# Kernel tuning notes

Hardware: AMD Instinct MI355X
Metric: run time of the kernel (lower is better)

The kernel has to match this reference:

```python
import jax, jax.numpy as jnp
import numpy as np

B, T, D, H = 8, 4096, 1024, 8
BW = D // H
MIN_DECAY = 0.001
EPS = 1e-05        # RGLRU eps (clamps)
SCAN_EPS = 1e-07   # closed_form_rnn_scan eps


def setup_inputs() -> dict:
    key = jax.random.key(0)
    k0, k1, k2 = jax.random.split(key, 3)
    x = jax.random.normal(k0, (B, T, D), dtype=jnp.float32)
    a_param = jnp.full((D,), -3.0, dtype=jnp.float32)
    # block-diagonal gate params (orthogonal-ish init approximated by scaled normal)
    w_in = jax.random.normal(k1, (H, BW, BW), dtype=jnp.float32) * (1.0 / np.sqrt(BW))
    b_in = jnp.ones((H, BW), dtype=jnp.float32)
    w_a = jax.random.normal(k2, (H, BW, BW), dtype=jnp.float32) * (1.0 / np.sqrt(BW))
    b_a = jnp.ones((H, BW), dtype=jnp.float32)
    return {"x": x, "a_param": a_param, "w_in": w_in, "b_in": b_in, "w_a": w_a, "b_a": b_a}


def block_diag_linear(x, w, b):
    # x: [B,T,D] -> [B,T,H,BW] ; w: [H,BW,BW] ; b: [H,BW]
    xb = x.reshape(x.shape[:-1] + (H, BW))
    y = jnp.einsum('bthi,hij->bthj', xb, w) + b
    return y.reshape(x.shape)


def closed_form_rnn_scan(x, a):
    # x, a: [B,T,D]; h0 = 0
    a_cumprod = jnp.cumprod(a, axis=1)
    ones = jnp.ones((x.shape[0], 1, x.shape[2]), dtype=x.dtype)
    p_prefix = jnp.concatenate([ones, a_cumprod[:, :-1, :]], axis=1)
    p_prefix = jnp.maximum(p_prefix, SCAN_EPS)
    w = (x + SCAN_EPS) / p_prefix
    S = jnp.cumsum(w, axis=1)
    h = p_prefix * S  # + p_prefix * h0 with h0 = 0
    return h, h[:, -1, :]


def reference(x, a_param, w_in, b_in, w_a, b_a):
    gate_x = jax.nn.sigmoid(block_diag_linear(x, w_in, b_in))
    gate_a = jax.nn.sigmoid(block_diag_linear(x, w_a, b_a))
    log_a = -gate_a * (jax.nn.softplus(a_param) + MIN_DECAY)
    a = jnp.minimum(jnp.exp(log_a), 1.0 - EPS)
    gated_x = x * gate_x
    multiplier = jnp.sqrt(jnp.maximum(1.0 - a * a, EPS))
    normed_x = gated_x * multiplier
    h, _ = closed_form_rnn_scan(normed_x, a)
    return h
```

## Files before the change

kernel.cpp:

```cpp
#include <hip/hip_runtime.h>

#define B_ 8
#define T_ 4096
#define D_ 1024
#define H_ 8
#define BW_ 128
#define NC_ 32
#define CT_ 128
#define EPS7 1e-7f
#define EPS5 1e-5f
#define LOG1MEPS -1.0000186e-05f

typedef _Float16 f16x8 __attribute__((ext_vector_type(8)));
typedef _Float16 f16x4 __attribute__((ext_vector_type(4)));
typedef float f32x4 __attribute__((ext_vector_type(4)));

__global__ __launch_bounds__(256) void k1_gates(
    const float* __restrict__ x, const float* __restrict__ a_param,
    const float* __restrict__ w_in, const float* __restrict__ b_in,
    const float* __restrict__ w_a, const float* __restrict__ b_a,
    float* __restrict__ Abuf, float* __restrict__ NX, float* __restrict__ CS)
{
  const int bid  = blockIdx.x;
  const int kc   = bid & (NC_ - 1);
  const int h    = (bid >> 5) & (H_ - 1);
  const int b    = bid >> 8;
  const int tid  = threadIdx.x;
  const int wave = tid >> 6;
  const int lane = tid & 63;
  const int quad = lane >> 4;
  const int l15  = lane & 15;

  __shared__ _Float16 xs[128 * 136];

  const float* xg = x + (size_t)(b * T_ + kc * CT_) * D_ + h * BW_;
  const int jc = wave * 32;

  f16x8 bf[2][2][4];
  #pragma unroll
  for (int g = 0; g < 2; ++g) {
    const float* wptr = (g ? w_a : w_in) + h * BW_ * BW_;
    #pragma unroll
    for (int jt = 0; jt < 2; ++jt) {
      #pragma unroll
      for (int k = 0; k < 4; ++k) {
        const float* wp = wptr + (k * 32 + quad * 8) * BW_ + jc + jt * 16 + l15;
        f16x8 f;
        #pragma unroll
        for (int i = 0; i < 8; ++i) f[i] = (_Float16)wp[i * BW_];
        bf[g][jt][k] = f;
      }
    }
  }
  float bI[2], bA[2], cdec[2];
  #pragma unroll
  for (int jt = 0; jt < 2; ++jt) {
    const int j = h * BW_ + jc + jt * 16 + l15;
    bI[jt] = b_in[j];
    bA[jt] = b_a[j];
    const float ap = a_param[j];
    cdec[jt] = ((ap > 20.f) ? ap : log1pf(__expf(ap))) + 0.001f;
  }

  {
    const int row = tid >> 1;
    const int cb  = (tid & 1) * 64;
    #pragma unroll
    for (int i = 0; i < 16; ++i) {
      const float4 v = *(const float4*)(xg + row * D_ + cb + i * 4);
      f16x4 hv = { (_Float16)v.x, (_Float16)v.y, (_Float16)v.z, (_Float16)v.w };
      *(f16x4*)(xs + row * 136 + cb + i * 4) = hv;
    }
  }
  __syncthreads();

  f32x4 acc[2][2][8];
  #pragma unroll
  for (int g = 0; g < 2; ++g)
    #pragma unroll
    for (int jt = 0; jt < 2; ++jt)
      #pragma unroll
      for (int m = 0; m < 8; ++m)
        acc[g][jt][m] = (f32x4){0.f, 0.f, 0.f, 0.f};

  #pragma unroll
  for (int m = 0; m < 8; ++m) {
    f16x8 af[4];
    #pragma unroll
    for (int k = 0; k < 4; ++k)
      af[k] = *(const f16x8*)(xs + (m * 16 + l15) * 136 + k * 32 + quad * 8);
    #pragma unroll
    for (int k = 0; k < 4; ++k)
      #pragma unroll
      for (int g = 0; g < 2; ++g)
        #pragma unroll
        for (int jt = 0; jt < 2; ++jt)
          acc[g][jt][m] = __builtin_amdgcn_mfma_f32_16x16x32_f16(
              af[k], bf[g][jt][k], acc[g][jt][m], 0, 0, 0);
  }

  float sla[2] = {0.f, 0.f};
  const size_t obase = (size_t)(b * T_ + kc * CT_) * D_ + h * BW_;
  #pragma unroll
  for (int m = 0; m < 8; ++m) {
    #pragma unroll
    for (int r = 0; r < 4; ++r) {
      const int row = m * 16 + quad * 4 + r;
      #pragma unroll
      for (int jt = 0; jt < 2; ++jt) {
        const int col = jc + jt * 16 + l15;
        const float yi = acc[0][jt][m][r] + bI[jt];
        const float ya = acc[1][jt][m][r] + bA[jt];
        const float gx = __builtin_amdgcn_rcpf(1.f + __expf(-yi));
        const float ga = __builtin_amdgcn_rcpf(1.f + __expf(-ya));
        const float la = -ga * cdec[jt];
        const float a  = fminf(__expf(la), 1.0f - EPS5);
        const float mult = sqrtf(fmaxf(fmaf(-a, a, 1.0f), EPS5));
        const float xval = xg[row * D_ + col];
        const float nx = xval * gx * mult;
        const size_t gi = obase + (size_t)row * D_ + col;
        Abuf[gi] = a;
        NX[gi]   = nx;
        sla[jt] += fminf(la, LOG1MEPS);
      }
    }
  }
  #pragma unroll
  for (int jt = 0; jt < 2; ++jt) {
    sla[jt] += __shfl_xor(sla[jt], 16, 64);
    sla[jt] += __shfl_xor(sla[jt], 32, 64);
  }
  if (quad == 0) {
    const int cs = (b * NC_ + kc) * D_ + h * BW_ + jc;
    CS[cs + l15]      = sla[0];
    CS[cs + 16 + l15] = sla[1];
  }
}

__global__ __launch_bounds__(256) void k2_scan_logs(float* __restrict__ CS)
{
  const int idx = blockIdx.x * 256 + threadIdx.x;
  const int b = idx >> 10;
  const int d = idx & (D_ - 1);
  float lq = 0.f;
  #pragma unroll
  for (int kk = 0; kk < NC_; ++kk) {
    const int o = (b * NC_ + kk) * D_ + d;
    const float c = CS[o];
    CS[o] = lq;
    lq += c;
  }
}

__device__ __forceinline__ float scan_r(float c, float pp, float aprev) {
  return (c > EPS7) ? aprev
                    : ((pp > EPS7) ? (EPS7 * __builtin_amdgcn_rcpf(pp)) : 1.0f);
}

__global__ __launch_bounds__(256) void k3_summary(
    const float* __restrict__ Abuf, const float* __restrict__ NX,
    const float* __restrict__ LQ, float* __restrict__ Ak, float* __restrict__ Bk)
{
  const int bid = blockIdx.x;
  const int g = bid & 3;
  const int k = (bid >> 2) & (NC_ - 1);
  const int b = bid >> 7;
  const int d = g * 256 + threadIdx.x;
  const int t0 = k * CT_;
  const size_t base = (size_t)(b * T_ + t0) * D_ + d;

  float c, pp, aprev;
  if (k == 0) { c = 1.f; pp = 1.f; aprev = 1.f; }
  else {
    c = __expf(LQ[(b * NC_ + k) * D_ + d]);
    aprev = Abuf[base - D_];
    pp = fmaxf(c / aprev, EPS7);
  }
  float hv = 0.f, rp = 1.f;
  for (int t = 0; t < CT_; t += 8) {
    float av[8], uv[8];
    #pragma unroll
    for (int i = 0; i < 8; ++i) {
      av[i] = Abuf[base + (size_t)(t + i) * D_];
      uv[i] = NX[base + (size_t)(t + i) * D_] + EPS7;
    }
    #pragma unroll
    for (int i = 0; i < 8; ++i) {
      const float p = fmaxf(c, EPS7);
      const float r = scan_r(c, pp, aprev);
      hv = fmaf(r, hv, uv[i]);
      rp *= r;
      c *= av[i]; pp = p; aprev = av[i];
    }
  }
  Ak[(b * NC_ + k) * D_ + d] = rp;
  Bk[(b * NC_ + k) * D_ + d] = hv;
}

__global__ __launch_bounds__(256) void k3_carry(
    float* __restrict__ Ak, const float* __restrict__ Bk)
{
  const int idx = blockIdx.x * 256 + threadIdx.x;
  const int b = idx >> 10;
  const int d = idx & (D_ - 1);
  float Hv = 0.f;
  #pragma unroll
  for (int kk = 0; kk < NC_; ++kk) {
    const int o = (b * NC_ + kk) * D_ + d;
    const float Av = Ak[o];
    Ak[o] = Hv;
    Hv = fmaf(Av, Hv, Bk[o]);
  }
}

__global__ __launch_bounds__(256) void k3_scan(
    const float* __restrict__ Abuf, float* NXO,
    const float* __restrict__ LQ, const float* __restrict__ Hc)
{
  const int bid = blockIdx.x;
  const int g = bid & 3;
  const int k = (bid >> 2) & (NC_ - 1);
  const int b = bid >> 7;
  const int d = g * 256 + threadIdx.x;
  const int t0 = k * CT_;
  const size_t base = (size_t)(b * T_ + t0) * D_ + d;

  float c, pp, aprev;
  if (k == 0) { c = 1.f; pp = 1.f; aprev = 1.f; }
  else {
    c = __expf(LQ[(b * NC_ + k) * D_ + d]);
    aprev = Abuf[base - D_];
    pp = fmaxf(c / aprev, EPS7);
  }
  float hv = Hc[(b * NC_ + k) * D_ + d];
  for (int t = 0; t < CT_; t += 8) {
    float av[8], uv[8];
    #pragma unroll
    for (int i = 0; i < 8; ++i) {
      av[i] = Abuf[base + (size_t)(t + i) * D_];
      uv[i] = NXO[base + (size_t)(t + i) * D_] + EPS7;
    }
    #pragma unroll
    for (int i = 0; i < 8; ++i) {
      const float p = fmaxf(c, EPS7);
      const float r = scan_r(c, pp, aprev);
      hv = fmaf(r, hv, uv[i]);
      NXO[base + (size_t)(t + i) * D_] = hv;
      c *= av[i]; pp = p; aprev = av[i];
    }
  }
}

extern "C" void kernel_launch(void* const* d_in, const int* in_sizes, int n_in,
                              void* d_out, int out_size, void* d_ws, size_t ws_size,
                              hipStream_t stream) {
  const float* x       = (const float*)d_in[0];
  const float* a_param = (const float*)d_in[1];
  const float* w_in    = (const float*)d_in[2];
  const float* b_in    = (const float*)d_in[3];
  const float* w_a     = (const float*)d_in[4];
  const float* b_a     = (const float*)d_in[5];
  float* out = (float*)d_out;

  char* ws = (char*)d_ws;
  float* Abuf = (float*)ws;
  float* CS   = (float*)(ws + (size_t)B_ * T_ * D_ * 4);
  float* Ak   = CS + B_ * NC_ * D_;
  float* Bk   = Ak + B_ * NC_ * D_;

  k1_gates<<<B_ * H_ * NC_, 256, 0, stream>>>(x, a_param, w_in, b_in, w_a, b_a,
                                              Abuf, out, CS);
  k2_scan_logs<<<(B_ * D_) / 256, 256, 0, stream>>>(CS);
  k3_summary<<<B_ * NC_ * (D_ / 256), 256, 0, stream>>>(Abuf, out, CS, Ak, Bk);
  k3_carry<<<(B_ * D_) / 256, 256, 0, stream>>>(Ak, Bk);
  k3_scan<<<B_ * NC_ * (D_ / 256), 256, 0, stream>>>(Abuf, out, CS, Ak);
}
```

Baseline: 434.5 us.

## Pack decay and normalized input into fp16 pairs, restructure gate kernel, prefetch scans

The gate kernel now stores one 32-bit word per element holding fp16 (1-a) and fp16 normalized input, in place of two fp32 arrays. This halves the intermediate traffic written by the gate kernel and read by both scan passes. The gate kernel also loops over column tiles to cut accumulator registers, targets 4 blocks per CU via launch bounds, and reads x from LDS rather than global memory. The scan kernels software-prefetch the next 8 timesteps. Storing these values in fp16 loses precision, and errors in a and the input can accumulate across the long recurrence.

```diff
diff --git a/kernel.cpp b/kernel.cpp
--- a/kernel.cpp
+++ b/kernel.cpp
@@ -1,4 +1,5 @@
 #include <hip/hip_runtime.h>
+#include <stdint.h>
 
 #define B_ 8
 #define T_ 4096
@@ -12,14 +13,29 @@
 #define LOG1MEPS -1.0000186e-05f
 
 typedef _Float16 f16x8 __attribute__((ext_vector_type(8)));
-typedef _Float16 f16x4 __attribute__((ext_vector_type(4)));
 typedef float f32x4 __attribute__((ext_vector_type(4)));
 
-__global__ __launch_bounds__(256) void k1_gates(
+__device__ __forceinline__ uint32_t pack_anx(float a, float nx) {
+  const unsigned short lo = __builtin_bit_cast(unsigned short, (_Float16)nx);
+  const unsigned short hi = __builtin_bit_cast(unsigned short, (_Float16)(1.0f - a));
+  return (uint32_t)lo | ((uint32_t)hi << 16);
+}
+__device__ __forceinline__ void unpack_anx(uint32_t v, float& a, float& u) {
+  const _Float16 lo = __builtin_bit_cast(_Float16, (unsigned short)(v & 0xffffu));
+  const _Float16 hi = __builtin_bit_cast(_Float16, (unsigned short)(v >> 16));
+  u = (float)lo + EPS7;
+  a = 1.0f - (float)hi;
+}
+__device__ __forceinline__ float unpack_a(uint32_t v) {
+  const _Float16 hi = __builtin_bit_cast(_Float16, (unsigned short)(v >> 16));
+  return 1.0f - (float)hi;
+}
+
+__global__ __launch_bounds__(256, 4) void k1_gates(
     const float* __restrict__ x, const float* __restrict__ a_param,
     const float* __restrict__ w_in, const float* __restrict__ b_in,
     const float* __restrict__ w_a, const float* __restrict__ b_a,
-    float* __restrict__ Abuf, float* __restrict__ NX, float* __restrict__ CS)
+    uint32_t* __restrict__ P, float* __restrict__ CS)
 {
   const int bid  = blockIdx.x;
   const int kc   = bid & (NC_ - 1);
@@ -36,91 +52,72 @@
   const float* xg = x + (size_t)(b * T_ + kc * CT_) * D_ + h * BW_;
   const int jc = wave * 32;
 
-  f16x8 bf[2][2][4];
-  #pragma unroll
-  for (int g = 0; g < 2; ++g) {
-    const float* wptr = (g ? w_a : w_in) + h * BW_ * BW_;
-    #pragma unroll
-    for (int jt = 0; jt < 2; ++jt) {
+  {
+    const int row   = tid & 127;
+    const int halfc = (tid >> 7) * 64;
+    const float*  xr = xg + (size_t)row * D_ + halfc;
+    _Float16*     xw = xs + row * 136 + halfc;
+    #pragma unroll
+    for (int i = 0; i < 8; ++i) {
+      const float4 v0 = *(const float4*)(xr + i * 8);
+      const float4 v1 = *(const float4*)(xr + i * 8 + 4);
+      f16x8 hv = { (_Float16)v0.x, (_Float16)v0.y, (_Float16)v0.z, (_Float16)v0.w,
+                   (_Float16)v1.x, (_Float16)v1.y, (_Float16)v1.z, (_Float16)v1.w };
+      *(f16x8*)(xw + i * 8) = hv;
+    }
+  }
+  __syncthreads();
+
+  float sla[2] = {0.f, 0.f};
+  const size_t obase = (size_t)(b * T_ + kc * CT_) * D_ + h * BW_;
+
+  for (int jt = 0; jt < 2; ++jt) {
+    const int col = jc + jt * 16 + l15;
+    const int jg  = h * BW_ + col;
+
+    f16x8 bf[2][4];
+    #pragma unroll
+    for (int g = 0; g < 2; ++g) {
+      const float* wptr = (g ? w_a : w_in) + h * BW_ * BW_ + col;
       #pragma unroll
       for (int k = 0; k < 4; ++k) {
-        const float* wp = wptr + (k * 32 + quad * 8) * BW_ + jc + jt * 16 + l15;
+        const float* wp = wptr + (k * 32 + quad * 8) * BW_;
         f16x8 f;
         #pragma unroll
         for (int i = 0; i < 8; ++i) f[i] = (_Float16)wp[i * BW_];
-        bf[g][jt][k] = f;
+        bf[g][k] = f;
       }
     }
-  }
-  float bI[2], bA[2], cdec[2];
-  #pragma unroll
-  for (int jt = 0; jt < 2; ++jt) {
-    const int j = h * BW_ + jc + jt * 16 + l15;
-    bI[jt] = b_in[j];
-    bA[jt] = b_a[j];
-    const float ap = a_param[j];
-    cdec[jt] = ((ap > 20.f) ? ap : log1pf(__expf(ap))) + 0.001f;
-  }
-
-  {
-    const int row = tid >> 1;
-    const int cb  = (tid & 1) * 64;
-    #pragma unroll
-    for (int i = 0; i < 16; ++i) {
-      const float4 v = *(const float4*)(xg + row * D_ + cb + i * 4);
-      f16x4 hv = { (_Float16)v.x, (_Float16)v.y, (_Float16)v.z, (_Float16)v.w };
-      *(f16x4*)(xs + row * 136 + cb + i * 4) = hv;
-    }
-  }
-  __syncthreads();
-
-  f32x4 acc[2][2][8];
-  #pragma unroll
-  for (int g = 0; g < 2; ++g)
-    #pragma unroll
-    for (int jt = 0; jt < 2; ++jt)
-      #pragma unroll
-      for (int m = 0; m < 8; ++m)
-        acc[g][jt][m] = (f32x4){0.f, 0.f, 0.f, 0.f};
-
-  #pragma unroll
-  for (int m = 0; m < 8; ++m) {
-    f16x8 af[4];
-    #pragma unroll
-    for (int k = 0; k < 4; ++k)
-      af[k] = *(const f16x8*)(xs + (m * 16 + l15) * 136 + k * 32 + quad * 8);
-    #pragma unroll
-    for (int k = 0; k < 4; ++k)
-      #pragma unroll
-      for (int g = 0; g < 2; ++g)
-        #pragma unroll
-        for (int jt = 0; jt < 2; ++jt)
-          acc[g][jt][m] = __builtin_amdgcn_mfma_f32_16x16x32_f16(
-              af[k], bf[g][jt][k], acc[g][jt][m], 0, 0, 0);
-  }
-
-  float sla[2] = {0.f, 0.f};
-  const size_t obase = (size_t)(b * T_ + kc * CT_) * D_ + h * BW_;
-  #pragma unroll
-  for (int m = 0; m < 8; ++m) {
-    #pragma unroll
-    for (int r = 0; r < 4; ++r) {
-      const int row = m * 16 + quad * 4 + r;
-      #pragma unroll
-      for (int jt = 0; jt < 2; ++jt) {
-        const int col = jc + jt * 16 + l15;
-        const float yi = acc[0][jt][m][r] + bI[jt];
-        const float ya = acc[1][jt][m][r] + bA[jt];
+    const float bI = b_in[jg];
+    const float bA = b_a[jg];
+    const float ap = a_param[jg];
+    const float cdec = ((ap > 20.f) ? ap : log1pf(__expf(ap))) + 0.001f;
+
+    #pragma unroll
+    for (int m = 0; m < 8; ++m) {
+      f16x8 af[4];
+      #pragma unroll
+      for (int k = 0; k < 4; ++k)
+        af[k] = *(const f16x8*)(xs + (m * 16 + l15) * 136 + k * 32 + quad * 8);
+      f32x4 accI = {0.f, 0.f, 0.f, 0.f}, accA = {0.f, 0.f, 0.f, 0.f};
+      #pragma unroll
+      for (int k = 0; k < 4; ++k) {
+        accI = __builtin_amdgcn_mfma_f32_16x16x32_f16(af[k], bf[0][k], accI, 0, 0, 0);
+        accA = __builtin_amdgcn_mfma_f32_16x16x32_f16(af[k], bf[1][k], accA, 0, 0, 0);
+      }
+      #pragma unroll
+      for (int r = 0; r < 4; ++r) {
+        const int row = m * 16 + quad * 4 + r;
+        const float yi = accI[r] + bI;
+        const float ya = accA[r] + bA;
         const float gx = __builtin_amdgcn_rcpf(1.f + __expf(-yi));
         const float ga = __builtin_amdgcn_rcpf(1.f + __expf(-ya));
-        const float la = -ga * cdec[jt];
+        const float la = -ga * cdec;
         const float a  = fminf(__expf(la), 1.0f - EPS5);
         const float mult = sqrtf(fmaxf(fmaf(-a, a, 1.0f), EPS5));
-        const float xval = xg[row * D_ + col];
-        const float nx = xval * gx * mult;
-        const size_t gi = obase + (size_t)row * D_ + col;
-        Abuf[gi] = a;
-        NX[gi]   = nx;
+        const float xv = (float)xs[row * 136 + col];
+        const float nx = xv * gx * mult;
+        P[obase + (size_t)row * D_ + col] = pack_anx(a, nx);
         sla[jt] += fminf(la, LOG1MEPS);
       }
     }
@@ -158,40 +155,44 @@
 }
 
 __global__ __launch_bounds__(256) void k3_summary(
-    const float* __restrict__ Abuf, const float* __restrict__ NX,
-    const float* __restrict__ LQ, float* __restrict__ Ak, float* __restrict__ Bk)
+    const uint32_t* __restrict__ P, const float* __restrict__ LQ,
+    float* __restrict__ Ak, float* __restrict__ Bk)
 {
   const int bid = blockIdx.x;
   const int g = bid & 3;
   const int k = (bid >> 2) & (NC_ - 1);
   const int b = bid >> 7;
   const int d = g * 256 + threadIdx.x;
-  const int t0 = k * CT_;
-  const size_t base = (size_t)(b * T_ + t0) * D_ + d;
+  const size_t base = (size_t)(b * T_ + k * CT_) * D_ + d;
 
   float c, pp, aprev;
   if (k == 0) { c = 1.f; pp = 1.f; aprev = 1.f; }
   else {
     c = __expf(LQ[(b * NC_ + k) * D_ + d]);
-    aprev = Abuf[base - D_];
+    aprev = unpack_a(P[base - D_]);
     pp = fmaxf(c / aprev, EPS7);
   }
+  uint32_t cur[8];
+  #pragma unroll
+  for (int i = 0; i < 8; ++i) cur[i] = P[base + (size_t)i * D_];
+
   float hv = 0.f, rp = 1.f;
   for (int t = 0; t < CT_; t += 8) {
-    float av[8], uv[8];
+    const int tn = (t + 8 < CT_) ? (t + 8) : t;
+    uint32_t nxt[8];
+    #pragma unroll
+    for (int i = 0; i < 8; ++i) nxt[i] = P[base + (size_t)(tn + i) * D_];
     #pragma unroll
     for (int i = 0; i < 8; ++i) {
-      av[i] = Abuf[base + (size_t)(t + i) * D_];
-      uv[i] = NX[base + (size_t)(t + i) * D_] + EPS7;
-    }
-    #pragma unroll
-    for (int i = 0; i < 8; ++i) {
+      float av, uv; unpack_anx(cur[i], av, uv);
       const float p = fmaxf(c, EPS7);
       const float r = scan_r(c, pp, aprev);
-      hv = fmaf(r, hv, uv[i]);
+      hv = fmaf(r, hv, uv);
       rp *= r;
-      c *= av[i]; pp = p; aprev = av[i];
-    }
+      c *= av; pp = p; aprev = av;
+    }
+    #pragma unroll
+    for (int i = 0; i < 8; ++i) cur[i] = nxt[i];
   }
   Ak[(b * NC_ + k) * D_ + d] = rp;
   Bk[(b * NC_ + k) * D_ + d] = hv;
@@ -214,40 +215,44 @@
 }
 
 __global__ __launch_bounds__(256) void k3_scan(
-    const float* __restrict__ Abuf, float* NXO,
-    const float* __restrict__ LQ, const float* __restrict__ Hc)
+    const uint32_t* __restrict__ P, const float* __restrict__ LQ,
+    const float* __restrict__ Hc, float* __restrict__ out)
 {
   const int bid = blockIdx.x;
   const int g = bid & 3;
   const int k = (bid >> 2) & (NC_ - 1);
   const int b = bid >> 7;
   const int d = g * 256 + threadIdx.x;
-  const int t0 = k * CT_;
-  const size_t base = (size_t)(b * T_ + t0) * D_ + d;
+  const size_t base = (size_t)(b * T_ + k * CT_) * D_ + d;
 
   float c, pp, aprev;
   if (k == 0) { c = 1.f; pp = 1.f; aprev = 1.f; }
   else {
     c = __expf(LQ[(b * NC_ + k) * D_ + d]);
-    aprev = Abuf[base - D_];
+    aprev = unpack_a(P[base - D_]);
     pp = fmaxf(c / aprev, EPS7);
   }
+  uint32_t cur[8];
+  #pragma unroll
+  for (int i = 0; i < 8; ++i) cur[i] = P[base + (size_t)i * D_];
+
   float hv = Hc[(b * NC_ + k) * D_ + d];
   for (int t = 0; t < CT_; t += 8) {
-    float av[8], uv[8];
+    const int tn = (t + 8 < CT_) ? (t + 8) : t;
+    uint32_t nxt[8];
+    #pragma unroll
+    for (int i = 0; i < 8; ++i) nxt[i] = P[base + (size_t)(tn + i) * D_];
     #pragma unroll
     for (int i = 0; i < 8; ++i) {
-      av[i] = Abuf[base + (size_t)(t + i) * D_];
-      uv[i] = NXO[base + (size_t)(t + i) * D_] + EPS7;
-    }
-    #pragma unroll
-    for (int i = 0; i < 8; ++i) {
+      float av, uv; unpack_anx(cur[i], av, uv);
       const float p = fmaxf(c, EPS7);
       const float r = scan_r(c, pp, aprev);
-      hv = fmaf(r, hv, uv[i]);
-      NXO[base + (size_t)(t + i) * D_] = hv;
-      c *= av[i]; pp = p; aprev = av[i];
-    }
+      hv = fmaf(r, hv, uv);
+      out[base + (size_t)(t + i) * D_] = hv;
+      c *= av; pp = p; aprev = av;
+    }
+    #pragma unroll
+    for (int i = 0; i < 8; ++i) cur[i] = nxt[i];
   }
 }
 
@@ -263,15 +268,15 @@
   float* out = (float*)d_out;
 
   char* ws = (char*)d_ws;
-  float* Abuf = (float*)ws;
-  float* CS   = (float*)(ws + (size_t)B_ * T_ * D_ * 4);
-  float* Ak   = CS + B_ * NC_ * D_;
-  float* Bk   = Ak + B_ * NC_ * D_;
+  uint32_t* P  = (uint32_t*)ws;
+  float*    CS = (float*)(ws + (size_t)B_ * T_ * D_ * 4);
+  float*    Ak = CS + B_ * NC_ * D_;
+  float*    Bk = Ak + B_ * NC_ * D_;
 
   k1_gates<<<B_ * H_ * NC_, 256, 0, stream>>>(x, a_param, w_in, b_in, w_a, b_a,
-                                              Abuf, out, CS);
+                                              P, CS);
   k2_scan_logs<<<(B_ * D_) / 256, 256, 0, stream>>>(CS);
-  k3_summary<<<B_ * NC_ * (D_ / 256), 256, 0, stream>>>(Abuf, out, CS, Ak, Bk);
+  k3_summary<<<B_ * NC_ * (D_ / 256), 256, 0, stream>>>(P, CS, Ak, Bk);
   k3_carry<<<(B_ * D_) / 256, 256, 0, stream>>>(Ak, Bk);
-  k3_scan<<<B_ * NC_ * (D_ / 256), 256, 0, stream>>>(Abuf, out, CS, Ak);
-}
+  k3_scan<<<B_ * NC_ * (D_ / 256), 256, 0, stream>>>(P, CS, Ak, out);
+}
```

After: 560.1 us. +28.9%, slower.
